# Kernel optimization log

Hardware: AMD Instinct MI355X
Metric: run time of the kernel (lower is better)

## Reference

```python
import jax, jax.numpy as jnp
import numpy as np

B, S, H = 4, 8256, 768
NH, HD = 12, 64
W = 128
SHIFT = W // 2  # 64; first SHIFT tokens form their own block after the shift
NW = (S - SHIFT) // W  # 64 full windows
ROPE_BASE = 10000.0


def _rope_cos_sin(length, hd):
    inv_freq = 1.0 / (ROPE_BASE ** (jnp.arange(0, hd, 2, dtype=jnp.float32) / hd))
    ang = jnp.arange(length, dtype=jnp.float32)[:, None] * inv_freq[None, :]  # [L, hd/2]
    return jnp.cos(ang), jnp.sin(ang)


def _apply_rope(x, cos, sin):
    # x: [..., L, hd]; cos/sin: [L, hd/2] (broadcast over leading dims)
    x1, x2 = x[..., : HD // 2], x[..., HD // 2 :]
    return jnp.concatenate([x1 * cos - x2 * sin, x2 * cos + x1 * sin], axis=-1)


def _sdpa(q, k, v):
    # q,k,v: [..., L, hd]; full softmax attention within the block
    scores = jnp.einsum('...qd,...kd->...qk', q, k) / jnp.sqrt(jnp.asarray(HD, q.dtype))
    probs = jax.nn.softmax(scores, axis=-1)
    return jnp.einsum('...qk,...kd->...qd', probs, v)


def setup_inputs() -> dict:
    key = jax.random.key(0)
    ks = jax.random.split(key, 8)
    std = 0.02
    return {
        'hidden_states': jax.random.normal(ks[0], (B, S, H), dtype=jnp.float32),
        'attention_mask': jnp.zeros((B, 1, 1, S), dtype=jnp.float32),
        'Wq': jax.random.normal(ks[1], (H, H), dtype=jnp.float32) * std,
        'bq': jnp.zeros((H,), dtype=jnp.float32),
        'Wk': jax.random.normal(ks[2], (H, H), dtype=jnp.float32) * std,
        'bk': jnp.zeros((H,), dtype=jnp.float32),
        'Wv': jax.random.normal(ks[3], (H, H), dtype=jnp.float32) * std,
        'bv': jnp.zeros((H,), dtype=jnp.float32),
    }


def _global_block(h, Wq, bq, Wk, bk, Wv, bv):
    # h: [B, L, H]; full attention with global-position RoPE (BertSelfAttention.forward)
    L = h.shape[1]
    cos, sin = _rope_cos_sin(L, HD)

    def heads(x):  # [B, L, H] -> [B, NH, L, HD]
        return x.reshape(B, L, NH, HD).transpose(0, 2, 1, 3)

    q = _apply_rope(heads(h @ Wq.T + bq), cos, sin)
    k = _apply_rope(heads(h @ Wk.T + bk), cos, sin)
    v = heads(h @ Wv.T + bv)
    ctx = _sdpa(q, k, v)  # [B, NH, L, HD]
    return ctx.transpose(0, 2, 1, 3).reshape(B, L, H)


def _local_blocks(h, Wq, bq, Wk, bk, Wv, bv):
    # h: [B, NW*W, H]; per-window attention with window-local RoPE (_mh_local)
    cos, sin = _rope_cos_sin(W, HD)

    def win_heads(x):  # [B, NW*W, H] -> [B, NW, NH, W, HD]
        return x.reshape(B, NW, W, NH, HD).transpose(0, 1, 3, 2, 4)

    q = _apply_rope(win_heads(h @ Wq.T + bq), cos, sin)
    k = _apply_rope(win_heads(h @ Wk.T + bk), cos, sin)
    v = win_heads(h @ Wv.T + bv)
    ctx = _sdpa(q, k, v)  # [B, NW, NH, W, HD]
    return ctx.transpose(0, 1, 3, 2, 4).reshape(B, NW * W, H)


def reference(hidden_states, attention_mask, Wq, bq, Wk, bk, Wv, bv):
    # Shifted local attention: first SHIFT tokens attend among themselves
    # (small global block), the rest is split into NW full windows of size W.
    head = _global_block(hidden_states[:, :SHIFT, :], Wq, bq, Wk, bk, Wv, bv)
    body = _local_blocks(hidden_states[:, SHIFT:, :], Wq, bq, Wk, bk, Wv, bv)
    return jnp.concatenate([head, body], axis=1)  # [B, S, H]
```

## Files before the change

### kernel.cpp

```cpp
#include <hip/hip_runtime.h>
#include <stdint.h>

constexpr int B  = 4, S = 8256, H = 768, NH = 12, HD = 64;
constexpr int M  = B * S;
constexpr int N3 = 3 * H;
constexpr int NWG_GEMM = (M / 128) * (N3 / 128);
constexpr int XQ8 = NWG_GEMM / 8, XR8 = NWG_GEMM % 8;
constexpr long XB_OFF   = 0;
constexpr long XB_BYTES = (long)M * H * 2;
constexpr long W_OFF    = XB_OFF + XB_BYTES;
constexpr long W_BYTES  = (long)N3 * H * 2;
constexpr long ROPE_OFF = W_OFF + W_BYTES;
constexpr long ROPE_BYTES = 128 * 32 * 2 * 4;
constexpr long QKV_OFF  = ROPE_OFF + ROPE_BYTES;
constexpr long QKV_BYTES = (long)M * N3 * 2;
constexpr long WS_NEEDED = QKV_OFF + QKV_BYTES;

typedef __attribute__((ext_vector_type(8))) _Float16 h8;
typedef __attribute__((ext_vector_type(8))) unsigned short us8;
typedef __attribute__((ext_vector_type(4))) float f4;

#define MFMA16(a,b,c) __builtin_amdgcn_mfma_f32_16x16x32_f16((a),(b),(c),0,0,0)
#define GLL16(gp, lp) __builtin_amdgcn_global_load_lds( \
    (__attribute__((address_space(1))) void*)(gp),      \
    (__attribute__((address_space(3))) void*)(lp), 16, 0, 0)

static __device__ __forceinline__ unsigned short f2h(float x) {
  _Float16 h = (_Float16)x;
  return __builtin_bit_cast(unsigned short, h);
}
static __device__ __forceinline__ f4 f4z() { f4 z = {0.f,0.f,0.f,0.f}; return z; }

__global__ __launch_bounds__(256) void prep_kernel(
    const float* __restrict__ X,
    const float* __restrict__ Wq, const float* __restrict__ Wk, const float* __restrict__ Wv,
    unsigned short* __restrict__ Xb, unsigned short* __restrict__ Wcat, float* __restrict__ rope)
{
  int bid = blockIdx.x;
  if (bid < 12384) {
    long base = (long)bid * 2048 + threadIdx.x * 8;
    float4 v0 = *(const float4*)(X + base);
    float4 v1 = *(const float4*)(X + base + 4);
    us8 o;
    o[0]=f2h(v0.x); o[1]=f2h(v0.y); o[2]=f2h(v0.z); o[3]=f2h(v0.w);
    o[4]=f2h(v1.x); o[5]=f2h(v1.y); o[6]=f2h(v1.z); o[7]=f2h(v1.w);
    *(us8*)(Xb + base) = o;
  } else if (bid < 13248) {
    int wb  = bid - 12384;
    int mat = wb / 288;
    int base = (wb % 288) * 2048 + threadIdx.x * 8;
    const float* src = (mat == 0) ? Wq : (mat == 1) ? Wk : Wv;
    float4 v0 = *(const float4*)(src + base);
    float4 v1 = *(const float4*)(src + base + 4);
    us8 o;
    o[0]=f2h(v0.x); o[1]=f2h(v0.y); o[2]=f2h(v0.z); o[3]=f2h(v0.w);
    o[4]=f2h(v1.x); o[5]=f2h(v1.y); o[6]=f2h(v1.z); o[7]=f2h(v1.w);
    *(us8*)(Wcat + (long)mat * 589824 + base) = o;
  } else {
    int t = (bid - 13248) * 256 + threadIdx.x;
    int p = t >> 5, i = t & 31;
    double ang = (double)p * pow(10000.0, -(double)i / 32.0);
    rope[2*t]   = (float)cos(ang);
    rope[2*t+1] = (float)sin(ang);
  }
}

__global__ __launch_bounds__(256) void qkv_gemm(
    const unsigned short* __restrict__ Xb, const unsigned short* __restrict__ Wb,
    const float* __restrict__ bqp, const float* __restrict__ bkp, const float* __restrict__ bvp,
    const float* __restrict__ rope, unsigned short* __restrict__ QKV)
{
  __shared__ __align__(16) unsigned char ldsA[2][16384];
  __shared__ __align__(16) unsigned char ldsB[2][16384];
  const int tid = threadIdx.x, lane = tid & 63, wid = tid >> 6;

  const int bid0 = blockIdx.x;
  const int xcd = bid0 & 7, idx = bid0 >> 3;
  const int wgid = (xcd < XR8 ? xcd * (XQ8 + 1) : XR8 * (XQ8 + 1) + (xcd - XR8) * XQ8) + idx;
  const int mt = wgid / 18;
  const int nt = wgid % 18;
  const long m0 = (long)mt * 128;
  const int  n0 = nt * 128;
  const int wm = wid >> 1, wn = wid & 1;

  f4 acc[4][4];
  #pragma unroll
  for (int i = 0; i < 4; ++i)
    #pragma unroll
    for (int j = 0; j < 4; ++j) acc[i][j] = f4z();

  const char* Xc = (const char*)Xb;
  const char* Wc = (const char*)Wb;

#define STAGE(Abuf, Bbuf, kt) do {                                          \
    const int k0b_ = (kt) * 128;                                            \
    _Pragma("unroll")                                                       \
    for (int i_ = 0; i_ < 4; ++i_) {                                        \
      const int ob_ = ((i_ << 2) + wid) * 1024;      \
      const int o_  = ob_ + lane * 16;                \
      const int row_ = o_ >> 7, cb_ = o_ & 127;                             \
      const int csrc_ = cb_ ^ ((row_ & 7) << 4);      \
      GLL16(Xc + (m0 + row_) * 1536 + k0b_ + csrc_, (Abuf) + ob_);          \
      GLL16(Wc + (long)(n0 + row_) * 1536 + k0b_ + csrc_, (Bbuf) + ob_);    \
    }                                                                       \
  } while (0)

#define COMPUTE(Abuf, Bbuf) do {                                            \
    _Pragma("unroll")                                                       \
    for (int ks_ = 0; ks_ < 2; ++ks_) {                                     \
      h8 a_[4], b_[4];                                                      \
      const int kb_ = ks_ * 64 + ((lane >> 4) << 4);                        \
      _Pragma("unroll")                                                     \
      for (int f_ = 0; f_ < 4; ++f_) {                                      \
        const int ra_ = wm * 64 + f_ * 16 + (lane & 15);                    \
        a_[f_] = *(const h8*)((Abuf) + ra_ * 128 + (kb_ ^ ((ra_ & 7) << 4)));\
        const int rb_ = wn * 64 + f_ * 16 + (lane & 15);                    \
        b_[f_] = *(const h8*)((Bbuf) + rb_ * 128 + (kb_ ^ ((rb_ & 7) << 4)));\
      }                                                                     \
      _Pragma("unroll")                                                     \
      for (int fm_ = 0; fm_ < 4; ++fm_)                                     \
        _Pragma("unroll")                                                   \
        for (int fn_ = 0; fn_ < 4; ++fn_)                                   \
          acc[fm_][fn_] = MFMA16(a_[fm_], b_[fn_], acc[fm_][fn_]);          \
    }                                                                       \
  } while (0)

  unsigned char* A0 = ldsA[0];  unsigned char* A1 = ldsA[1];
  unsigned char* B0 = ldsB[0];  unsigned char* B1 = ldsB[1];

  STAGE(A0, B0, 0);
  #pragma unroll
  for (int kt = 0; kt < 12; kt += 2) {
    STAGE(A1, B1, kt + 1);
    asm volatile("s_waitcnt vmcnt(8)" ::: "memory");
    __builtin_amdgcn_s_barrier();
    asm volatile("" ::: "memory");
    COMPUTE(A0, B0);
    asm volatile("" ::: "memory");
    __builtin_amdgcn_s_barrier();
    if (kt + 2 < 12) {
      STAGE(A0, B0, kt + 2);
      asm volatile("s_waitcnt vmcnt(8)" ::: "memory");
    } else {
      asm volatile("s_waitcnt vmcnt(0)" ::: "memory");
    }
    __builtin_amdgcn_s_barrier();
    asm volatile("" ::: "memory");
    COMPUTE(A1, B1);
    asm volatile("" ::: "memory");
    __builtin_amdgcn_s_barrier();
  }
#undef STAGE
#undef COMPUTE

  const int colb = n0 + wn * 64;
  const int sel = (colb >= 1536) ? 2 : (colb >= 768) ? 1 : 0;
  const float* bias = (sel == 0) ? bqp : (sel == 1) ? bkp : bvp;
  const int hcol = colb % 768;
  float bia[4];
  #pragma unroll
  for (int f = 0; f < 4; ++f) bia[f] = bias[hcol + f * 16 + (lane & 15)];

  #pragma unroll
  for (int fm = 0; fm < 4; ++fm) {
    #pragma unroll
    for (int reg = 0; reg < 4; ++reg) {
      const long m = m0 + wm * 64 + fm * 16 + ((lane >> 4) << 2) + reg;
      const int s = (int)(m % (long)S);
      const int pos = (s < 64) ? s : ((s - 64) & 127);
      unsigned short* orow = QKV + m * N3 + colb;
      if (sel < 2) {
        #pragma unroll
        for (int f = 0; f < 2; ++f) {
          const int d1 = f * 16 + (lane & 15);
          const float c  = rope[(pos * 32 + d1) * 2];
          const float sn = rope[(pos * 32 + d1) * 2 + 1];
          const float x1 = acc[fm][f][reg]     + bia[f];
          const float x2 = acc[fm][f + 2][reg] + bia[f + 2];
          orow[f * 16 + (lane & 15)]       = f2h(x1 * c - x2 * sn);
          orow[(f + 2) * 16 + (lane & 15)] = f2h(x2 * c + x1 * sn);
        }
      } else {
        #pragma unroll
        for (int f = 0; f < 4; ++f)
          orow[f * 16 + (lane & 15)] = f2h(acc[fm][f][reg] + bia[f]);
      }
    }
  }
}

template <int T>
__global__ __launch_bounds__(256) void attn_kernel(
    const unsigned short* __restrict__ QKV, float* __restrict__ out)
{
  constexpr int NF  = T / 16;
  constexpr int NKS = T / 32;
  __shared__ __align__(16) unsigned char sVT[16384];
  __shared__ __align__(16) unsigned char sP[4][8192];

  const int tid = threadIdx.x, lane = tid & 63, w = tid >> 6;
  int bid = blockIdx.x;
  const int h = bid % NH; bid /= NH;
  long row0;
  if (T == 64) row0 = (long)bid * S;
  else { const int ww = bid % 64; const int b = bid / 64; row0 = (long)b * S + 64 + (long)ww * 128; }
  const unsigned short* Qb = QKV + row0 * N3 + h * HD;
  const unsigned short* Kb = Qb + H;
  const unsigned short* Vb = Qb + 2 * H;

  {
    const int p = lane;
    if (2 * p + 1 < T) {
      const unsigned short* v0 = Vb + (long)(2 * p) * N3 + w * 16;
      const unsigned short* v1 = v0 + N3;
      us8 a0 = *(const us8*)(v0);
      us8 a1 = *(const us8*)(v0 + 8);
      us8 c0 = *(const us8*)(v1);
      us8 c1 = *(const us8*)(v1 + 8);
      #pragma unroll
      for (int i = 0; i < 8; ++i) {
        const int d = w * 16 + i, d2 = d + 8;
        *(unsigned*)(sVT + d  * 256 + ((4 * p) ^ ((d  & 15) << 4))) = (unsigned)a0[i] | ((unsigned)c0[i] << 16);
        *(unsigned*)(sVT + d2 * 256 + ((4 * p) ^ ((d2 & 15) << 4))) = (unsigned)a1[i] | ((unsigned)c1[i] << 16);
      }
    }
  }
  __syncthreads();

  if (w * 32 < T) {
    h8 aq[2][2];
    #pragma unroll
    for (int fm = 0; fm < 2; ++fm)
      #pragma unroll
      for (int ks = 0; ks < 2; ++ks) {
        const long r = w * 32 + fm * 16 + (lane & 15);
        aq[fm][ks] = *(const h8*)(Qb + r * N3 + ks * 32 + ((lane >> 4) << 3));
      }

    f4 acc[2][NF];
    #pragma unroll
    for (int i = 0; i < 2; ++i)
      #pragma unroll
      for (int f = 0; f < NF; ++f) acc[i][f] = f4z();

    #pragma unroll
    for (int f = 0; f < NF; ++f) {
      const long rk = f * 16 + (lane & 15);
      const unsigned short* kr = Kb + rk * N3 + ((lane >> 4) << 3);
      h8 b0 = *(const h8*)(kr);
      h8 b1 = *(const h8*)(kr + 32);
      acc[0][f] = MFMA16(aq[0][0], b0, acc[0][f]);
      acc[0][f] = MFMA16(aq[0][1], b1, acc[0][f]);
      acc[1][f] = MFMA16(aq[1][0], b0, acc[1][f]);
      acc[1][f] = MFMA16(aq[1][1], b1, acc[1][f]);
    }

    unsigned char* Pw = sP[w];
    #pragma unroll
    for (int fm = 0; fm < 2; ++fm) {
      #pragma unroll
      for (int reg = 0; reg < 4; ++reg) {
        float mx = -3.0e38f;
        #pragma unroll
        for (int f = 0; f < NF; ++f) mx = fmaxf(mx, acc[fm][f][reg]);
        mx = fmaxf(mx, __shfl_xor(mx, 1));
        mx = fmaxf(mx, __shfl_xor(mx, 2));
        mx = fmaxf(mx, __shfl_xor(mx, 4));
        mx = fmaxf(mx, __shfl_xor(mx, 8));
        float pv[NF], sum = 0.f;
        #pragma unroll
        for (int f = 0; f < NF; ++f) {
          const float p = __expf((acc[fm][f][reg] - mx) * 0.125f);
          pv[f] = p; sum += p;
        }
        sum += __shfl_xor(sum, 1);
        sum += __shfl_xor(sum, 2);
        sum += __shfl_xor(sum, 4);
        sum += __shfl_xor(sum, 8);
        const float inv = 1.0f / sum;
        const int rloc = fm * 16 + ((lane >> 4) << 2) + reg;
        const int swz = (rloc & 7) << 4;
        #pragma unroll
        for (int f = 0; f < NF; ++f) {
          const int cb = (f * 16 + (lane & 15)) * 2;
          *(unsigned short*)(Pw + rloc * 256 + (cb ^ swz)) = f2h(pv[f] * inv);
        }
      }
    }

    f4 acc2[2][4];
    #pragma unroll
    for (int i = 0; i < 2; ++i)
      #pragma unroll
      for (int j = 0; j < 4; ++j) acc2[i][j] = f4z();

    #pragma unroll
    for (int ks = 0; ks < NKS; ++ks) {
      h8 pa[2], vb[4];
      const int kb = ks * 64 + ((lane >> 4) << 4);
      #pragma unroll
      for (int fm = 0; fm < 2; ++fm) {
        const int rp = fm * 16 + (lane & 15);
        pa[fm] = *(const h8*)(Pw + rp * 256 + (kb ^ ((rp & 7) << 4)));
      }
      #pragma unroll
      for (int df = 0; df < 4; ++df) {
        const int d = df * 16 + (lane & 15);
        vb[df] = *(const h8*)(sVT + d * 256 + (kb ^ ((d & 15) << 4)));
      }
      #pragma unroll
      for (int fm = 0; fm < 2; ++fm)
        #pragma unroll
        for (int df = 0; df < 4; ++df)
          acc2[fm][df] = MFMA16(pa[fm], vb[df], acc2[fm][df]);
    }

    float* ob = out + (row0 + w * 32) * H + h * HD;
    #pragma unroll
    for (int fm = 0; fm < 2; ++fm)
      #pragma unroll
      for (int df = 0; df < 4; ++df)
        #pragma unroll
        for (int reg = 0; reg < 4; ++reg) {
          const long r = fm * 16 + ((lane >> 4) << 2) + reg;
          const int c = df * 16 + (lane & 15);
          ob[r * H + c] = acc2[fm][df][reg];
        }
  }
}

extern "C" void kernel_launch(void* const* d_in, const int* in_sizes, int n_in,
                              void* d_out, int out_size, void* d_ws, size_t ws_size,
                              hipStream_t stream) {
  const float* X  = (const float*)d_in[0];
  const float* Wq = (const float*)d_in[2];
  const float* bq = (const float*)d_in[3];
  const float* Wk = (const float*)d_in[4];
  const float* bk = (const float*)d_in[5];
  const float* Wv = (const float*)d_in[6];
  const float* bv = (const float*)d_in[7];
  float* out = (float*)d_out;

  if ((long)ws_size < WS_NEEDED) return;

  char* ws = (char*)d_ws;
  unsigned short* Xb   = (unsigned short*)(ws + XB_OFF);
  unsigned short* Wcat = (unsigned short*)(ws + W_OFF);
  float*          rope = (float*)(ws + ROPE_OFF);
  unsigned short* QKV  = (unsigned short*)(ws + QKV_OFF);

  prep_kernel<<<13264, 256, 0, stream>>>(X, Wq, Wk, Wv, Xb, Wcat, rope);
  qkv_gemm<<<NWG_GEMM, 256, 0, stream>>>(Xb, Wcat, bq, bk, bv, rope, QKV);
  attn_kernel<64><<<B * NH, 256, 0, stream>>>(QKV, out);
  attn_kernel<128><<<B * 64 * NH, 256, 0, stream>>>(QKV, out);
}
```

Before: 418.0 us.

## Enlarge QKV GEMM tile to 256x256 with eight waves and unified LDS

The QKV projection GEMM moves from 128x128 tiles with 4 waves to 256x256 tiles with 8 waves (512 threads). Each wave now accumulates a 128x64 sub-tile, and A and B are staged into a single 64KB double-buffered LDS region. The workgroup order is also changed so tiles that share the same weight columns run together. The goal is more data reuse per byte loaded from global memory and fewer tiles overall. The costs are 128KB of LDS and many more accumulator registers per workgroup, which lowers occupancy and leaves a coarser tail of 1161 workgroups.

```diff
diff --git a/kernel.cpp b/kernel.cpp
--- a/kernel.cpp
+++ b/kernel.cpp
@@ -4,7 +4,9 @@
 constexpr int B  = 4, S = 8256, H = 768, NH = 12, HD = 64;
 constexpr int M  = B * S;
 constexpr int N3 = 3 * H;
-constexpr int NWG_GEMM = (M / 128) * (N3 / 128);
+constexpr int MT = M / 256;
+constexpr int NT = N3 / 256;
+constexpr int NWG_GEMM = MT * NT;
 constexpr int XQ8 = NWG_GEMM / 8, XR8 = NWG_GEMM % 8;
 constexpr long XB_OFF   = 0;
 constexpr long XB_BYTES = (long)M * H * 2;
@@ -65,88 +67,96 @@
   }
 }
 
-__global__ __launch_bounds__(256) void qkv_gemm(
+__global__ __launch_bounds__(512, 2) void qkv_gemm(
     const unsigned short* __restrict__ Xb, const unsigned short* __restrict__ Wb,
     const float* __restrict__ bqp, const float* __restrict__ bkp, const float* __restrict__ bvp,
     const float* __restrict__ rope, unsigned short* __restrict__ QKV)
 {
-  __shared__ __align__(16) unsigned char ldsA[2][16384];
-  __shared__ __align__(16) unsigned char ldsB[2][16384];
+  __shared__ __align__(16) unsigned char lds[2][65536];
   const int tid = threadIdx.x, lane = tid & 63, wid = tid >> 6;
 
   const int bid0 = blockIdx.x;
   const int xcd = bid0 & 7, idx = bid0 >> 3;
   const int wgid = (xcd < XR8 ? xcd * (XQ8 + 1) : XR8 * (XQ8 + 1) + (xcd - XR8) * XQ8) + idx;
-  const int mt = wgid / 18;
-  const int nt = wgid % 18;
-  const long m0 = (long)mt * 128;
-  const int  n0 = nt * 128;
-  const int wm = wid >> 1, wn = wid & 1;
-
-  f4 acc[4][4];
+  const int nt = wgid / MT;
+  const int mt = wgid % MT;
+  const long m0 = (long)mt * 256;
+  const int  n0 = nt * 256;
+  const int wm = wid >> 2, wn = wid & 3;
+
+  f4 acc[8][4];
   #pragma unroll
-  for (int i = 0; i < 4; ++i)
+  for (int i = 0; i < 8; ++i)
     #pragma unroll
     for (int j = 0; j < 4; ++j) acc[i][j] = f4z();
 
   const char* Xc = (const char*)Xb;
   const char* Wc = (const char*)Wb;
 
-#define STAGE(Abuf, Bbuf, kt) do {                                          \
+#define STAGE(buf, kt) do {                                                 \
     const int k0b_ = (kt) * 128;                                            \
     _Pragma("unroll")                                                       \
-    for (int i_ = 0; i_ < 4; ++i_) {                                        \
-      const int ob_ = ((i_ << 2) + wid) * 1024;      \
+    for (int i_ = 0; i_ < 8; ++i_) {                                        \
+      const int ob_ = i_ * 8192 + wid * 1024;        \
       const int o_  = ob_ + lane * 16;                \
-      const int row_ = o_ >> 7, cb_ = o_ & 127;                             \
-      const int csrc_ = cb_ ^ ((row_ & 7) << 4);      \
-      GLL16(Xc + (m0 + row_) * 1536 + k0b_ + csrc_, (Abuf) + ob_);          \
-      GLL16(Wc + (long)(n0 + row_) * 1536 + k0b_ + csrc_, (Bbuf) + ob_);    \
+      if (i_ < 4) {                                 \
+        const int row_ = o_ >> 7, cb_ = o_ & 127;                           \
+        const int csrc_ = cb_ ^ ((row_ & 7) << 4);                          \
+        GLL16(Xc + (m0 + row_) * 1536 + k0b_ + csrc_, (buf) + ob_);         \
+      } else {                                    \
+        const int o2_ = o_ - 32768;                                         \
+        const int row_ = o2_ >> 7, cb_ = o2_ & 127;                         \
+        const int csrc_ = cb_ ^ ((row_ & 7) << 4);                          \
+        GLL16(Wc + (long)(n0 + row_) * 1536 + k0b_ + csrc_, (buf) + ob_);   \
+      }                                                                     \
     }                                                                       \
   } while (0)
 
-#define COMPUTE(Abuf, Bbuf) do {                                            \
+#define COMPUTE(buf) do {                                                   \
     _Pragma("unroll")                                                       \
     for (int ks_ = 0; ks_ < 2; ++ks_) {                                     \
-      h8 a_[4], b_[4];                                                      \
+      h8 a_[8], b_[4];                                                      \
       const int kb_ = ks_ * 64 + ((lane >> 4) << 4);                        \
       _Pragma("unroll")                                                     \
-      for (int f_ = 0; f_ < 4; ++f_) {                                      \
-        const int ra_ = wm * 64 + f_ * 16 + (lane & 15);                    \
-        a_[f_] = *(const h8*)((Abuf) + ra_ * 128 + (kb_ ^ ((ra_ & 7) << 4)));\
-        const int rb_ = wn * 64 + f_ * 16 + (lane & 15);                    \
-        b_[f_] = *(const h8*)((Bbuf) + rb_ * 128 + (kb_ ^ ((rb_ & 7) << 4)));\
+      for (int f_ = 0; f_ < 8; ++f_) {                                      \
+        const int ra_ = wm * 128 + f_ * 16 + (lane & 15);                   \
+        a_[f_] = *(const h8*)((buf) + ra_ * 128 + (kb_ ^ ((ra_ & 7) << 4)));\
       }                                                                     \
       _Pragma("unroll")                                                     \
-      for (int fm_ = 0; fm_ < 4; ++fm_)                                     \
+      for (int f_ = 0; f_ < 4; ++f_) {                                      \
+        const int rb_ = wn * 64 + f_ * 16 + (lane & 15);                    \
+        b_[f_] = *(const h8*)((buf) + 32768 + rb_ * 128 + (kb_ ^ ((rb_ & 7) << 4))); \
+      }                                                                     \
+      _Pragma("unroll")                                                     \
+      for (int fm_ = 0; fm_ < 8; ++fm_)                                     \
         _Pragma("unroll")                                                   \
         for (int fn_ = 0; fn_ < 4; ++fn_)                                   \
           acc[fm_][fn_] = MFMA16(a_[fm_], b_[fn_], acc[fm_][fn_]);          \
     }                                                                       \
   } while (0)
 
-  unsigned char* A0 = ldsA[0];  unsigned char* A1 = ldsA[1];
-  unsigned char* B0 = ldsB[0];  unsigned char* B1 = ldsB[1];
-
-  STAGE(A0, B0, 0);
+  unsigned char* L0 = lds[0];
+  unsigned char* L1 = lds[1];
+
+  STAGE(L0, 0);
   #pragma unroll
   for (int kt = 0; kt < 12; kt += 2) {
-    STAGE(A1, B1, kt + 1);
+    STAGE(L1, kt + 1);
     asm volatile("s_waitcnt vmcnt(8)" ::: "memory");
     __builtin_amdgcn_s_barrier();
     asm volatile("" ::: "memory");
-    COMPUTE(A0, B0);
+    COMPUTE(L0);
     asm volatile("" ::: "memory");
     __builtin_amdgcn_s_barrier();
     if (kt + 2 < 12) {
-      STAGE(A0, B0, kt + 2);
+      STAGE(L0, kt + 2);
       asm volatile("s_waitcnt vmcnt(8)" ::: "memory");
     } else {
       asm volatile("s_waitcnt vmcnt(0)" ::: "memory");
     }
     __builtin_amdgcn_s_barrier();
     asm volatile("" ::: "memory");
-    COMPUTE(A1, B1);
+    COMPUTE(L1);
     asm volatile("" ::: "memory");
     __builtin_amdgcn_s_barrier();
   }
@@ -162,10 +172,10 @@
   for (int f = 0; f < 4; ++f) bia[f] = bias[hcol + f * 16 + (lane & 15)];
 
   #pragma unroll
-  for (int fm = 0; fm < 4; ++fm) {
+  for (int fm = 0; fm < 8; ++fm) {
     #pragma unroll
     for (int reg = 0; reg < 4; ++reg) {
-      const long m = m0 + wm * 64 + fm * 16 + ((lane >> 4) << 2) + reg;
+      const long m = m0 + wm * 128 + fm * 16 + ((lane >> 4) << 2) + reg;
       const int s = (int)(m % (long)S);
       const int pos = (s < 64) ? s : ((s - 64) & 127);
       unsigned short* orow = QKV + m * N3 + colb;
@@ -350,7 +360,7 @@
   unsigned short* QKV  = (unsigned short*)(ws + QKV_OFF);
 
   prep_kernel<<<13264, 256, 0, stream>>>(X, Wq, Wk, Wv, Xb, Wcat, rope);
-  qkv_gemm<<<NWG_GEMM, 256, 0, stream>>>(Xb, Wcat, bq, bk, bv, rope, QKV);
+  qkv_gemm<<<NWG_GEMM, 512, 0, stream>>>(Xb, Wcat, bq, bk, bv, rope, QKV);
   attn_kernel<64><<<B * NH, 256, 0, stream>>>(QKV, out);
   attn_kernel<128><<<B * 64 * NH, 256, 0, stream>>>(QKV, out);
 }
```

Measured after the change: 412.2 us. About the same (-1.4%).
